# Performance work log

Measured on AMD Instinct MI355X. Metric: run time of the kernel, lower is better.

## Reference

```python
import jax, jax.numpy as jnp
import numpy as np

NMS_THRESH = 0.3  # default nms_thresh in DetNet.predict


def setup_inputs() -> dict:
    key = jax.random.key(0)
    k1, k2, k3, k4 = jax.random.split(key, 4)
    W, N = 8, 1024
    det = jax.random.uniform(k1, (W, N, 5), dtype=jnp.float32)          # (conf, cx, cy, w, h) in [0,1)
    offsets = jax.random.uniform(k2, (W, 5), dtype=jnp.float32) * 0.5   # window offset vector (0, left, top, 0, 0)-like
    scales = jax.random.uniform(k3, (W, 5), dtype=jnp.float32) * 0.5 + 0.25  # window scale vector
    b = jax.random.uniform(k4, (W, 4), dtype=jnp.float32)
    # (valid_left, valid_right, valid_top, valid_bottom) with left<right, top<bottom
    bounds = jnp.stack([0.3 * b[:, 0], 0.7 + 0.3 * b[:, 1],
                        0.3 * b[:, 2], 0.7 + 0.3 * b[:, 3]], axis=-1)
    return {"det": det, "offsets": offsets, "scales": scales, "bounds": bounds}


def _pairwise_iou(boxes):
    # boxes: [M,4] in (x1,y1,x2,y2)
    x1, y1, x2, y2 = boxes[:, 0], boxes[:, 1], boxes[:, 2], boxes[:, 3]
    area = jnp.clip(x2 - x1, 0.0) * jnp.clip(y2 - y1, 0.0)              # [M]
    iw = jnp.clip(jnp.minimum(x2[:, None], x2[None, :]) - jnp.maximum(x1[:, None], x1[None, :]), 0.0)
    ih = jnp.clip(jnp.minimum(y2[:, None], y2[None, :]) - jnp.maximum(y1[:, None], y1[None, :]), 0.0)
    inter = iw * ih                                                     # [M,M]
    union = area[:, None] + area[None, :] - inter
    return inter / jnp.maximum(union, 1e-9)


def reference(det, offsets, scales, bounds):
    W, N, _ = det.shape
    M = W * N
    cx, cy = det[..., 1], det[..., 2]                                    # [W,N]
    left, right = bounds[:, 0:1], bounds[:, 1:2]
    top, bottom = bounds[:, 2:3], bounds[:, 3:4]
    valid = (cx < right) & (cx > left) & (cy < bottom) & (cy > top)      # [W,N] border mask
    # torch.addcmul(offset, d, scale) = offset + d * scale
    d = (offsets[:, None, :] + det * scales[:, None, :]).reshape(M, 5)
    valid = valid.reshape(M)
    scores = jnp.where(valid, d[:, 0], -1.0)                             # invalid boxes never kept
    order = jnp.argsort(-scores)                                         # descending confidence
    d_s = d[order]                                                       # [M,5]
    s_s = scores[order]
    # point_form: (cx,cy,w,h) -> (x1,y1,x2,y2)
    cxy, wh = d_s[:, 1:3], d_s[:, 3:5]
    boxes = jnp.concatenate([cxy - wh * 0.5, cxy + wh * 0.5], axis=-1)
    iou = jax.lax.stop_gradient(_pairwise_iou(boxes))                    # [M,M], suppression is non-diff
    s_c = jax.lax.stop_gradient(s_s)
    idx = jnp.arange(M)

    def body(i, keep):
        # suppressed if any kept higher-score box overlaps > thresh
        sup = jnp.any(keep & (idx < i) & (iou[:, i] > NMS_THRESH))
        return keep.at[i].set(jnp.logical_and(~sup, s_c[i] > 0.0))

    keep = jax.lax.fori_loop(0, M, body, jnp.ones((M,), dtype=bool))
    return d_s * keep[:, None].astype(d_s.dtype)                         # [M,5], suppressed rows zeroed
```

## Files before the change

kernel.cpp:

```cpp
#include <hip/hip_runtime.h>
#include <cstdint>


#define M_TOT 8192
#define NMS_T 0.3f

#define WS_BOX   65536
#define WS_D     196608
#define WS_VCNT  360448
#define WS_ZROW  393216
#define WS_DONE  458752
#define WS_MASK  524288

typedef unsigned long long u64t;

__device__ __forceinline__ uint32_t desc_key(float sv) {
    uint32_t u = __float_as_uint(sv);
    uint32_t m = (u & 0x80000000u) ? ~u : (u | 0x80000000u);
    return ~m;
}
__device__ __forceinline__ u64t rdl64(u64t v, int sl) {
    unsigned lo = (unsigned)__builtin_amdgcn_readlane((int)(unsigned)v, sl);
    unsigned hi = (unsigned)__builtin_amdgcn_readlane((int)(unsigned)(v >> 32), sl);
    return ((u64t)hi << 32) | lo;
}
__device__ __forceinline__ u64t rdfl64(u64t v) {
    unsigned lo = (unsigned)__builtin_amdgcn_readfirstlane((int)(unsigned)v);
    unsigned hi = (unsigned)__builtin_amdgcn_readfirstlane((int)(unsigned)(v >> 32));
    return ((u64t)hi << 32) | lo;
}

__device__ __forceinline__ void scatter_one(
    int i, int rank, u64t key,
    const float* __restrict__ det, const float* __restrict__ offsets,
    const float* __restrict__ scales,
    float4* __restrict__ boxes_srt, float* __restrict__ d_srt)
{
    uint32_t dkey = (uint32_t)(key >> 16);
    if (dkey >= 0x7FFFFFFFu) return;
    int g = i >> 10;
    float d0 = __fadd_rn(offsets[g*5+0], __fmul_rn(det[i*5+0], scales[g*5+0]));
    float d1 = __fadd_rn(offsets[g*5+1], __fmul_rn(det[i*5+1], scales[g*5+1]));
    float d2 = __fadd_rn(offsets[g*5+2], __fmul_rn(det[i*5+2], scales[g*5+2]));
    float d3 = __fadd_rn(offsets[g*5+3], __fmul_rn(det[i*5+3], scales[g*5+3]));
    float d4 = __fadd_rn(offsets[g*5+4], __fmul_rn(det[i*5+4], scales[g*5+4]));
    d_srt[rank*5+0] = d0; d_srt[rank*5+1] = d1; d_srt[rank*5+2] = d2;
    d_srt[rank*5+3] = d3; d_srt[rank*5+4] = d4;
    float hw = __fmul_rn(d3, 0.5f), hh = __fmul_rn(d4, 0.5f);
    boxes_srt[rank] = make_float4(__fsub_rn(d1, hw), __fsub_rn(d2, hh),
                                  __fadd_rn(d1, hw), __fadd_rn(d2, hh));
}

__global__ __launch_bounds__(512) void k2_rank(
    const float* __restrict__ det, const float* __restrict__ offsets,
    const float* __restrict__ scales, const float* __restrict__ bounds,
    float4* __restrict__ boxes_srt, float* __restrict__ d_srt,
    unsigned int* __restrict__ vcnt, u64t* __restrict__ zrow,
    unsigned int* __restrict__ done, float* __restrict__ out)
{
    __shared__ u64t skey[M_TOT];
    __shared__ float soff[40], sscl[40], sbnd[32];
    __shared__ int sTop;
    int t = threadIdx.x;
    int lane = t & 63;
    if (t == 0) sTop = 0;
    if (t < 40) { soff[t] = offsets[t]; sscl[t] = scales[t]; }
    if (t < 32) { sbnd[t] = bounds[t]; }
    if (blockIdx.x == 0 && t < 128) zrow[t] = 0ull;
    if (blockIdx.x == 0 && t < 64)  done[t] = 0u;
    __syncthreads();

    #pragma unroll 4
    for (int s = 0; s < 16; ++s) {
        int u = s * 512 + t;
        int g = u >> 10;
        float raw_s = det[u * 5 + 0];
        float cx    = det[u * 5 + 1];
        float cy    = det[u * 5 + 2];
        float score = __fadd_rn(soff[g * 5 + 0], __fmul_rn(raw_s, sscl[g * 5 + 0]));
        bool valid = (cx < sbnd[g*4+1]) && (cx > sbnd[g*4+0]) &&
                     (cy < sbnd[g*4+3]) && (cy > sbnd[g*4+2]);
        float sv = valid ? score : -1.0f;
        uint32_t dk = desc_key(sv);
        bool push = dk < 0x7FFFFFFFu;
        u64t key = ((u64t)dk << 16) | (unsigned)u;
        u64t bal = __ballot(push);
        if (bal) {
            int lw = 0;
            if (lane == 0) lw = atomicAdd(&sTop, __popcll(bal));
            int wbase = __builtin_amdgcn_readfirstlane(lw);
            if (push) {
                int off = __popcll(bal & ((1ull << lane) - 1ull));
                skey[wbase + off] = key;
            }
        }
    }
    __syncthreads();
    int V = sTop;
    int Vpad = (V + 15) & ~15;
    if (t < Vpad - V) skey[V + t] = ~0ull;
    {
        int zb = blockIdx.x * 320;
        for (int z = zb + t; z < zb + 320; z += 512) out[z] = 0.0f;
    }
    __syncthreads();
    if (t == 0) *vcnt = (unsigned)V;

    int grp = t >> 3;
    int jq  = t & 7;
    int i = blockIdx.x * 64 + grp;
    int g = i >> 10;
    float raw_s = det[i * 5 + 0];
    float cx    = det[i * 5 + 1];
    float cy    = det[i * 5 + 2];
    float score = __fadd_rn(soff[g * 5 + 0], __fmul_rn(raw_s, sscl[g * 5 + 0]));
    bool valid = (cx < sbnd[g*4+1]) && (cx > sbnd[g*4+0]) &&
                 (cy < sbnd[g*4+3]) && (cy > sbnd[g*4+2]);
    float sv = valid ? score : -1.0f;
    uint32_t dk = desc_key(sv);
    u64t ki = ((u64t)dk << 16) | (unsigned)i;
    const ulonglong2* skey2 = (const ulonglong2*)skey;
    int c = 0;
    int nit = Vpad >> 4;
    #pragma unroll 4
    for (int it = 0; it < nit; ++it) {
        ulonglong2 kj = skey2[it * 8 + jq];
        c += (kj.x < ki) + (kj.y < ki);
    }
    c += __shfl_xor(c, 1);
    c += __shfl_xor(c, 2);
    c += __shfl_xor(c, 4);
    if (jq == 0)
        scatter_one(i, c, ki, det, offsets, scales, boxes_srt, d_srt);
}

__global__ __launch_bounds__(512) void k34_fused(
    const float4* __restrict__ boxes_srt,
    const u64t* __restrict__ zrow,
    const float* __restrict__ d_srt,
    const unsigned int* __restrict__ vcnt,
    u64t* __restrict__ mask,
    unsigned int* __restrict__ done,
    float* __restrict__ out)
{
    int V = (int)*vcnt;
    int nwords = (V + 63) >> 6;
    int nc = (V + 127) >> 7;
    int tid = threadIdx.x;

    if (blockIdx.x != 0) {
        __shared__ float4 sb[8 * 65];
        __shared__ float  sa[8 * 65];
        int b = (int)blockIdx.x - 1;
        int gpre = 0;
        for (int c = 0; c < nc; ++c) {
            int w0 = 2 * c;
            int Wc = nwords - w0;
            int tiles = 2 * ((Wc + 7) >> 3);
            int tau0 = ((b - gpre) % 127 + 127) % 127;
            for (int tau = tau0; tau < tiles; tau += 127) {
                int rt = tau & 1, wt = tau >> 1;
                int rowbase = c * 128 + rt * 64;
                int wbase = w0 + wt * 8;
                {
                    int u = tid;
                    float4 bb = boxes_srt[min(wbase * 64 + u, M_TOT - 1)];
                    int cc = u >> 6, jj = u & 63;
                    sb[cc * 65 + jj] = bb;
                    sa[cc * 65 + jj] = __fmul_rn(fmaxf(__fsub_rn(bb.z, bb.x), 0.0f),
                                                 fmaxf(__fsub_rn(bb.w, bb.y), 0.0f));
                }
                __syncthreads();
                int r  = rowbase + (tid >> 3);
                int wl = tid & 7;
                int w  = wbase + wl;
                if (r < V && w < nwords) {
                    float4 bi = boxes_srt[r];
                    float ai = __fmul_rn(fmaxf(__fsub_rn(bi.z, bi.x), 0.0f),
                                         fmaxf(__fsub_rn(bi.w, bi.y), 0.0f));
                    u64t bits = 0;
                    #pragma unroll 4
                    for (int jj = 0; jj < 64; ++jj) {
                        float4 bj = sb[wl * 65 + jj];
                        float aj = sa[wl * 65 + jj];
                        float iw = fmaxf(__fsub_rn(fminf(bi.z, bj.z), fmaxf(bi.x, bj.x)), 0.0f);
                        float ih = fmaxf(__fsub_rn(fminf(bi.w, bj.w), fmaxf(bi.y, bj.y)), 0.0f);
                        float inter = __fmul_rn(iw, ih);
                        float uni   = __fsub_rn(__fadd_rn(ai, aj), inter);
                        float iou   = __fdiv_rn(inter, fmaxf(uni, 1e-9f));
                        int j = w * 64 + jj;
                        if (j > r && iou > NMS_T) bits |= 1ull << jj;
                    }
                    mask[(size_t)r * 128 + w] = bits;
                }
                __syncthreads();
                if (tid == 0) {
                    int rows_t  = V - rowbase; if (rows_t > 64) rows_t = 64;
                    int words_t = nwords - wbase; if (words_t > 8) words_t = 8;
                    if (rows_t > 0) {
                        __threadfence();
                        __hip_atomic_fetch_add(&done[c], (unsigned)(rows_t * words_t),
                                               __ATOMIC_RELEASE, __HIP_MEMORY_SCOPE_AGENT);
                    }
                }
                __syncthreads();
            }
            gpre += tiles;
        }
        return;
    }

    __shared__ u64t sdead[128];
    __shared__ u64t ck[128];
    __shared__ int  res_prog;
    __shared__ int  h_prog[7];
    int wv = tid >> 6, lane = tid & 63;

    if (tid < 128) {
        int bw = tid * 64;
        u64t w0v = 0;
        if (bw >= V)           w0v = ~0ull;
        else if (bw + 64 > V)  w0v = (~0ull) << (V - bw);
        sdead[tid] = w0v;
        ck[tid] = 0ull;
    }
    if (tid == 0) res_prog = 0;
    if (tid < 7)  h_prog[tid] = tid;
    __syncthreads();

    if (wv == 0) {
        if (nc > 0) {
            u64t cA_lo = 0, cA_hi = 0;
            {
                int rows_c = V; if (rows_c > 128) rows_c = 128;
                unsigned expc = (unsigned)(rows_c * nwords);
                while (__hip_atomic_load(&done[0], __ATOMIC_RELAXED, __HIP_MEMORY_SCOPE_AGENT) < expc)
                    __builtin_amdgcn_s_sleep(2);
                (void)__hip_atomic_load(&done[0], __ATOMIC_ACQUIRE, __HIP_MEMORY_SCOPE_AGENT);
            }
            ulonglong2 bl, bln, bh, bhn;
            {
                int rl = min(lane,      M_TOT - 1);
                int rh = min(64 + lane, M_TOT - 1);
                const u64t* rpl = mask + (size_t)rl * 128;
                const u64t* rph = mask + (size_t)rh * 128;
                bl  = *(const ulonglong2*)(rpl);
                bln = *(const ulonglong2*)(rpl + 2);
                bh  = *(const ulonglong2*)(rph);
                bhn = *(const ulonglong2*)(rph + 2);
            }
            for (int T = 0; T < nc; ++T) {
                ulonglong2 nbl, nbln, nbh, nbhn;
                bool havenext = (T + 1 < nc);
                if (havenext) {
                    int c = T + 1;
                    int rows_c = V - c * 128; if (rows_c > 128) rows_c = 128;
                    unsigned expc = (unsigned)(rows_c * (nwords - 2 * c));
                    while (__hip_atomic_load(&done[c], __ATOMIC_RELAXED, __HIP_MEMORY_SCOPE_AGENT) < expc)
                        __builtin_amdgcn_s_sleep(2);
                    (void)__hip_atomic_load(&done[c], __ATOMIC_ACQUIRE, __HIP_MEMORY_SCOPE_AGENT);
                    int rl = min(c * 128 + lane,      M_TOT - 1);
                    int rh = min(c * 128 + 64 + lane, M_TOT - 1);
                    int w = min(2 * c, 124);
                    const u64t* rpl = mask + (size_t)rl * 128;
                    const u64t* rph = mask + (size_t)rh * 128;
                    nbl  = *(const ulonglong2*)(rpl + w);
                    nbln = *(const ulonglong2*)(rpl + w + 2);
                    nbh  = *(const ulonglong2*)(rph + w);
                    nbhn = *(const ulonglong2*)(rph + w + 2);
                }
                if (T >= 2) {
                    int need = T - 1;
                    while (true) {
                        int hp = (lane < 7) ? ((volatile int*)h_prog)[lane] : 0x7FFFFFFF;
                        if (__ballot(hp < need) == 0ull) break;
                    }
                }
                u64t dlo = rdfl64(((volatile u64t*)sdead)[2 * T]);
                u64t dhi = rdfl64(((volatile u64t*)sdead)[2 * T + 1]);
                u64t live_lo = ~(dlo | cA_lo);
                u64t live_hi = ~(dhi | cA_hi);
                int rem = V - T * 128;
                if (rem < 128) {
                    live_lo &= (rem >= 64) ? ~0ull : ((rem <= 0) ? 0ull : ((1ull << rem) - 1ull));
                    int rh = rem - 64;
                    live_hi &= (rh >= 64) ? ~0ull : ((rh <= 0) ? 0ull : ((1ull << rh) - 1ull));
                }
                u64t km_lo = 0, km_hi = 0;
                while (live_lo) {
                    int bs = (int)__builtin_ctzll(live_lo);
                    km_lo |= 1ull << bs;
                    u64t rml = rdl64(bl.x, bs);
                    u64t rmh = rdl64(bl.y, bs);
                    live_lo &= ~rml & ~(1ull << bs);
                    live_hi &= ~rmh;
                }
                while (live_hi) {
                    int bs = (int)__builtin_ctzll(live_hi);
                    km_hi |= 1ull << bs;
                    u64t rmh = rdl64(bh.y, bs);
                    live_hi &= ~rmh & ~(1ull << bs);
                }
                if (lane == 0) { ck[2 * T] = km_lo; ck[2 * T + 1] = km_hi; }
                __threadfence_block();
                if (lane == 0) *(volatile int*)&res_prog = T + 1;
                u64t c1l = 0, c1h = 0, km = km_lo;
                while (km) {
                    int b_ = (int)__builtin_ctzll(km); km &= km - 1;
                    c1l |= rdl64(bln.x, b_); c1h |= rdl64(bln.y, b_);
                }
                km = km_hi;
                while (km) {
                    int b_ = (int)__builtin_ctzll(km); km &= km - 1;
                    c1l |= rdl64(bhn.x, b_); c1h |= rdl64(bhn.y, b_);
                }
                cA_lo = c1l; cA_hi = c1h;
                if (havenext) { bl = nbl; bln = nbln; bh = nbh; bhn = nbhn; }
            }
        }
    } else {
        int hh = wv - 1;
        for (int c = hh; c < nc; c += 7) {
            while (*(volatile int*)&res_prog <= c) __builtin_amdgcn_s_sleep(1);
            (void)__hip_atomic_load(&done[c], __ATOMIC_ACQUIRE, __HIP_MEMORY_SCOPE_AGENT);
            u64t kl = ((volatile u64t*)ck)[2 * c];
            u64t kh = ((volatile u64t*)ck)[2 * c + 1];
            if (kl | kh) {
                int base = c * 128;
                u64t ax = 0, ay = 0;
                while (kl | kh) {
                    ulonglong2 bq[4];
                    #pragma unroll
                    for (int q = 0; q < 4; ++q) {
                        const ulonglong2* ptr;
                        if (kl) {
                            int b_ = __builtin_ctzll(kl); kl &= kl - 1;
                            ptr = (const ulonglong2*)(mask + (size_t)(base + b_) * 128) + lane;
                        } else if (kh) {
                            int b_ = __builtin_ctzll(kh); kh &= kh - 1;
                            ptr = (const ulonglong2*)(mask + (size_t)(base + 64 + b_) * 128) + lane;
                        } else {
                            ptr = (const ulonglong2*)zrow + lane;
                        }
                        bq[q] = *ptr;
                    }
                    ax |= bq[0].x | bq[1].x | bq[2].x | bq[3].x;
                    ay |= bq[0].y | bq[1].y | bq[2].y | bq[3].y;
                }
                atomicOr(&sdead[2 * lane],     ax);
                atomicOr(&sdead[2 * lane + 1], ay);
            }
            __threadfence_block();
            if (lane == 0) ((volatile int*)h_prog)[hh] = c + 7;
        }
        if (lane == 0) ((volatile int*)h_prog)[hh] = 0x7FFFFFFF;
    }
    __syncthreads();
    if (tid < 128) {
        u64t m = ck[tid];
        while (m) {
            int b_ = __builtin_ctzll(m); m &= m - 1;
            int rr = tid * 64 + b_;
            out[rr * 5 + 0] = d_srt[rr * 5 + 0];
            out[rr * 5 + 1] = d_srt[rr * 5 + 1];
            out[rr * 5 + 2] = d_srt[rr * 5 + 2];
            out[rr * 5 + 3] = d_srt[rr * 5 + 3];
            out[rr * 5 + 4] = d_srt[rr * 5 + 4];
        }
    }
}

extern "C" void kernel_launch(void* const* d_in, const int* in_sizes, int n_in,
                              void* d_out, int out_size, void* d_ws, size_t ws_size,
                              hipStream_t stream) {
    const float* det     = (const float*)d_in[0];
    const float* offsets = (const float*)d_in[1];
    const float* scales  = (const float*)d_in[2];
    const float* bounds  = (const float*)d_in[3];
    float* out = (float*)d_out;
    char* ws = (char*)d_ws;
    float4*       boxes = (float4*)(ws + WS_BOX);
    float*        d_srt = (float*)(ws + WS_D);
    unsigned int* vcnt  = (unsigned int*)(ws + WS_VCNT);
    u64t*         zrow  = (u64t*)(ws + WS_ZROW);
    unsigned int* done  = (unsigned int*)(ws + WS_DONE);
    u64t*         mask  = (u64t*)(ws + WS_MASK);

    k2_rank<<<128, 512, 0, stream>>>(det, offsets, scales, bounds, boxes, d_srt, vcnt, zrow, done, out);
    k34_fused<<<128, 512, 0, stream>>>(boxes, zrow, d_srt, vcnt, mask, done, out);
}
```

Before: 138.7 us.

## Build diagonal mask tiles first and signal them with separate per-chunk counters

Worker blocks now compute the diagonal (wt==0) mask tiles for every chunk before any off-diagonal tiles. Each diagonal tile bumps a new doneD counter, so the resolver wave only waits on diagonal completion instead of the whole chunk row. The helper waves that OR suppression rows now spin on the full done counter themselves. This lets the serial resolve chain start earlier and overlap with off-diagonal mask construction, at the cost of extra atomics and a changed tile schedule.

```diff
diff --git a/kernel.cpp b/kernel.cpp
--- a/kernel.cpp
+++ b/kernel.cpp
@@ -10,6 +10,7 @@
 #define WS_VCNT  360448
 #define WS_ZROW  393216
 #define WS_DONE  458752
+#define WS_DONED 459008
 #define WS_MASK  524288
 
 typedef unsigned long long u64t;
@@ -56,7 +57,8 @@
     const float* __restrict__ scales, const float* __restrict__ bounds,
     float4* __restrict__ boxes_srt, float* __restrict__ d_srt,
     unsigned int* __restrict__ vcnt, u64t* __restrict__ zrow,
-    unsigned int* __restrict__ done, float* __restrict__ out)
+    unsigned int* __restrict__ done, unsigned int* __restrict__ doneD,
+    float* __restrict__ out)
 {
     __shared__ u64t skey[M_TOT];
     __shared__ float soff[40], sscl[40], sbnd[32];
@@ -67,7 +69,7 @@
     if (t < 40) { soff[t] = offsets[t]; sscl[t] = scales[t]; }
     if (t < 32) { sbnd[t] = bounds[t]; }
     if (blockIdx.x == 0 && t < 128) zrow[t] = 0ull;
-    if (blockIdx.x == 0 && t < 64)  done[t] = 0u;
+    if (blockIdx.x == 0 && t < 64)  { done[t] = 0u; doneD[t] = 0u; }
     __syncthreads();
 
     #pragma unroll 4
@@ -134,6 +136,61 @@
         scatter_one(i, c, ki, det, offsets, scales, boxes_srt, d_srt);
 }
 
+__device__ __forceinline__ void build_tile(
+    int c, int rt, int wt, int V, int nwords,
+    const float4* __restrict__ boxes_srt, u64t* __restrict__ mask,
+    unsigned int* __restrict__ done, unsigned int* __restrict__ doneD,
+    float4* sb, float* sa, int tid)
+{
+    int rowbase = c * 128 + rt * 64;
+    int wbase = 2 * c + wt * 8;
+    {
+        int u = tid;
+        float4 bb = boxes_srt[min(wbase * 64 + u, M_TOT - 1)];
+        int cc = u >> 6, jj = u & 63;
+        sb[cc * 65 + jj] = bb;
+        sa[cc * 65 + jj] = __fmul_rn(fmaxf(__fsub_rn(bb.z, bb.x), 0.0f),
+                                     fmaxf(__fsub_rn(bb.w, bb.y), 0.0f));
+    }
+    __syncthreads();
+    int r  = rowbase + (tid >> 3);
+    int wl = tid & 7;
+    int w  = wbase + wl;
+    if (r < V && w < nwords) {
+        float4 bi = boxes_srt[r];
+        float ai = __fmul_rn(fmaxf(__fsub_rn(bi.z, bi.x), 0.0f),
+                             fmaxf(__fsub_rn(bi.w, bi.y), 0.0f));
+        u64t bits = 0;
+        #pragma unroll 4
+        for (int jj = 0; jj < 64; ++jj) {
+            float4 bj = sb[wl * 65 + jj];
+            float aj = sa[wl * 65 + jj];
+            float iw = fmaxf(__fsub_rn(fminf(bi.z, bj.z), fmaxf(bi.x, bj.x)), 0.0f);
+            float ih = fmaxf(__fsub_rn(fminf(bi.w, bj.w), fmaxf(bi.y, bj.y)), 0.0f);
+            float inter = __fmul_rn(iw, ih);
+            float uni   = __fsub_rn(__fadd_rn(ai, aj), inter);
+            float iou   = __fdiv_rn(inter, fmaxf(uni, 1e-9f));
+            int j = w * 64 + jj;
+            if (j > r && iou > NMS_T) bits |= 1ull << jj;
+        }
+        mask[(size_t)r * 128 + w] = bits;
+    }
+    __syncthreads();
+    if (tid == 0) {
+        int rows_t  = V - rowbase; if (rows_t > 64) rows_t = 64;
+        int words_t = nwords - wbase; if (words_t > 8) words_t = 8;
+        if (rows_t > 0) {
+            __threadfence();
+            __hip_atomic_fetch_add(&done[c], (unsigned)(rows_t * words_t),
+                                   __ATOMIC_RELEASE, __HIP_MEMORY_SCOPE_AGENT);
+            if (wt == 0)
+                __hip_atomic_fetch_add(&doneD[c], 1u,
+                                       __ATOMIC_RELEASE, __HIP_MEMORY_SCOPE_AGENT);
+        }
+    }
+    __syncthreads();
+}
+
 __global__ __launch_bounds__(512) void k34_fused(
     const float4* __restrict__ boxes_srt,
     const u64t* __restrict__ zrow,
@@ -141,6 +198,7 @@
     const unsigned int* __restrict__ vcnt,
     u64t* __restrict__ mask,
     unsigned int* __restrict__ done,
+    unsigned int* __restrict__ doneD,
     float* __restrict__ out)
 {
     int V = (int)*vcnt;
@@ -152,58 +210,19 @@
         __shared__ float4 sb[8 * 65];
         __shared__ float  sa[8 * 65];
         int b = (int)blockIdx.x - 1;
+        for (int d = b; d < 2 * nc; d += 127) {
+            build_tile(d >> 1, d & 1, 0, V, nwords,
+                       boxes_srt, mask, done, doneD, sb, sa, tid);
+        }
         int gpre = 0;
         for (int c = 0; c < nc; ++c) {
-            int w0 = 2 * c;
-            int Wc = nwords - w0;
-            int tiles = 2 * ((Wc + 7) >> 3);
+            int Wc = nwords - 2 * c;
+            int octets = (Wc + 7) >> 3;
+            int tiles = 2 * (octets - 1);
             int tau0 = ((b - gpre) % 127 + 127) % 127;
             for (int tau = tau0; tau < tiles; tau += 127) {
-                int rt = tau & 1, wt = tau >> 1;
-                int rowbase = c * 128 + rt * 64;
-                int wbase = w0 + wt * 8;
-                {
-                    int u = tid;
-                    float4 bb = boxes_srt[min(wbase * 64 + u, M_TOT - 1)];
-                    int cc = u >> 6, jj = u & 63;
-                    sb[cc * 65 + jj] = bb;
-                    sa[cc * 65 + jj] = __fmul_rn(fmaxf(__fsub_rn(bb.z, bb.x), 0.0f),
-                                                 fmaxf(__fsub_rn(bb.w, bb.y), 0.0f));
-                }
-                __syncthreads();
-                int r  = rowbase + (tid >> 3);
-                int wl = tid & 7;
-                int w  = wbase + wl;
-                if (r < V && w < nwords) {
-                    float4 bi = boxes_srt[r];
-                    float ai = __fmul_rn(fmaxf(__fsub_rn(bi.z, bi.x), 0.0f),
-                                         fmaxf(__fsub_rn(bi.w, bi.y), 0.0f));
-                    u64t bits = 0;
-                    #pragma unroll 4
-                    for (int jj = 0; jj < 64; ++jj) {
-                        float4 bj = sb[wl * 65 + jj];
-                        float aj = sa[wl * 65 + jj];
-                        float iw = fmaxf(__fsub_rn(fminf(bi.z, bj.z), fmaxf(bi.x, bj.x)), 0.0f);
-                        float ih = fmaxf(__fsub_rn(fminf(bi.w, bj.w), fmaxf(bi.y, bj.y)), 0.0f);
-                        float inter = __fmul_rn(iw, ih);
-                        float uni   = __fsub_rn(__fadd_rn(ai, aj), inter);
-                        float iou   = __fdiv_rn(inter, fmaxf(uni, 1e-9f));
-                        int j = w * 64 + jj;
-                        if (j > r && iou > NMS_T) bits |= 1ull << jj;
-                    }
-                    mask[(size_t)r * 128 + w] = bits;
-                }
-                __syncthreads();
-                if (tid == 0) {
-                    int rows_t  = V - rowbase; if (rows_t > 64) rows_t = 64;
-                    int words_t = nwords - wbase; if (words_t > 8) words_t = 8;
-                    if (rows_t > 0) {
-                        __threadfence();
-                        __hip_atomic_fetch_add(&done[c], (unsigned)(rows_t * words_t),
-                                               __ATOMIC_RELEASE, __HIP_MEMORY_SCOPE_AGENT);
-                    }
-                }
-                __syncthreads();
+                build_tile(c, tau & 1, (tau >> 1) + 1, V, nwords,
+                           boxes_srt, mask, done, doneD, sb, sa, tid);
             }
             gpre += tiles;
         }
@@ -233,10 +252,10 @@
             u64t cA_lo = 0, cA_hi = 0;
             {
                 int rows_c = V; if (rows_c > 128) rows_c = 128;
-                unsigned expc = (unsigned)(rows_c * nwords);
-                while (__hip_atomic_load(&done[0], __ATOMIC_RELAXED, __HIP_MEMORY_SCOPE_AGENT) < expc)
+                unsigned expd = (rows_c > 64) ? 2u : 1u;
+                while (__hip_atomic_load(&doneD[0], __ATOMIC_RELAXED, __HIP_MEMORY_SCOPE_AGENT) < expd)
                     __builtin_amdgcn_s_sleep(2);
-                (void)__hip_atomic_load(&done[0], __ATOMIC_ACQUIRE, __HIP_MEMORY_SCOPE_AGENT);
+                (void)__hip_atomic_load(&doneD[0], __ATOMIC_ACQUIRE, __HIP_MEMORY_SCOPE_AGENT);
             }
             ulonglong2 bl, bln, bh, bhn;
             {
@@ -255,10 +274,10 @@
                 if (havenext) {
                     int c = T + 1;
                     int rows_c = V - c * 128; if (rows_c > 128) rows_c = 128;
-                    unsigned expc = (unsigned)(rows_c * (nwords - 2 * c));
-                    while (__hip_atomic_load(&done[c], __ATOMIC_RELAXED, __HIP_MEMORY_SCOPE_AGENT) < expc)
+                    unsigned expd = (rows_c > 64) ? 2u : 1u;
+                    while (__hip_atomic_load(&doneD[c], __ATOMIC_RELAXED, __HIP_MEMORY_SCOPE_AGENT) < expd)
                         __builtin_amdgcn_s_sleep(2);
-                    (void)__hip_atomic_load(&done[c], __ATOMIC_ACQUIRE, __HIP_MEMORY_SCOPE_AGENT);
+                    (void)__hip_atomic_load(&doneD[c], __ATOMIC_ACQUIRE, __HIP_MEMORY_SCOPE_AGENT);
                     int rl = min(c * 128 + lane,      M_TOT - 1);
                     int rh = min(c * 128 + 64 + lane, M_TOT - 1);
                     int w = min(2 * c, 124);
@@ -322,7 +341,13 @@
         int hh = wv - 1;
         for (int c = hh; c < nc; c += 7) {
             while (*(volatile int*)&res_prog <= c) __builtin_amdgcn_s_sleep(1);
-            (void)__hip_atomic_load(&done[c], __ATOMIC_ACQUIRE, __HIP_MEMORY_SCOPE_AGENT);
+            {
+                int rows_c = V - c * 128; if (rows_c > 128) rows_c = 128;
+                unsigned expc = (unsigned)(rows_c * (nwords - 2 * c));
+                while (__hip_atomic_load(&done[c], __ATOMIC_RELAXED, __HIP_MEMORY_SCOPE_AGENT) < expc)
+                    __builtin_amdgcn_s_sleep(1);
+                (void)__hip_atomic_load(&done[c], __ATOMIC_ACQUIRE, __HIP_MEMORY_SCOPE_AGENT);
+            }
             u64t kl = ((volatile u64t*)ck)[2 * c];
             u64t kh = ((volatile u64t*)ck)[2 * c + 1];
             if (kl | kh) {
@@ -384,8 +409,11 @@
     unsigned int* vcnt  = (unsigned int*)(ws + WS_VCNT);
     u64t*         zrow  = (u64t*)(ws + WS_ZROW);
     unsigned int* done  = (unsigned int*)(ws + WS_DONE);
+    unsigned int* doneD = (unsigned int*)(ws + WS_DONED);
     u64t*         mask  = (u64t*)(ws + WS_MASK);
 
-    k2_rank<<<128, 512, 0, stream>>>(det, offsets, scales, bounds, boxes, d_srt, vcnt, zrow, done, out);
-    k34_fused<<<128, 512, 0, stream>>>(boxes, zrow, d_srt, vcnt, mask, done, out);
-}
+    k2_rank<<<128, 512, 0, stream>>>(det, offsets, scales, bounds, boxes, d_srt,
+                                     vcnt, zrow, done, doneD, out);
+    k34_fused<<<dim3(128), 512, 0, stream>>>(boxes, zrow, d_srt, vcnt, mask,
+                                             done, doneD, out);
+}
```

Result: slower. 144.6 us (+4.2%).

## Replace multi-wave NMS resolve pipeline with single-wave register-resident dead mask

Applied to the files above, without the earlier changes.

The serial NMS resolve stage moves from a one-resolver-plus-seven-helper-wavefront scheme, which coordinated through shared memory progress flags and atomics, to a single wavefront. That wavefront keeps the accumulated suppression bitmask in registers (two u64 per lane) and ORs in the mask rows of kept boxes itself. Output rows for kept boxes are written inline, so the final block-wide scatter pass is gone. This removes cross-wave spin-waiting, LDS atomics and the early next-tile lookahead (cA), at the cost of making the resolver wave do all mask-row loads serially on its critical path.

```diff
diff --git a/kernel.cpp b/kernel.cpp
--- a/kernel.cpp
+++ b/kernel.cpp
@@ -22,11 +22,6 @@
 __device__ __forceinline__ u64t rdl64(u64t v, int sl) {
     unsigned lo = (unsigned)__builtin_amdgcn_readlane((int)(unsigned)v, sl);
     unsigned hi = (unsigned)__builtin_amdgcn_readlane((int)(unsigned)(v >> 32), sl);
-    return ((u64t)hi << 32) | lo;
-}
-__device__ __forceinline__ u64t rdfl64(u64t v) {
-    unsigned lo = (unsigned)__builtin_amdgcn_readfirstlane((int)(unsigned)v);
-    unsigned hi = (unsigned)__builtin_amdgcn_readfirstlane((int)(unsigned)(v >> 32));
     return ((u64t)hi << 32) | lo;
 }
 
@@ -210,163 +205,91 @@
         return;
     }
 
-    __shared__ u64t sdead[128];
-    __shared__ u64t ck[128];
-    __shared__ int  res_prog;
-    __shared__ int  h_prog[7];
-    int wv = tid >> 6, lane = tid & 63;
-
-    if (tid < 128) {
-        int bw = tid * 64;
-        u64t w0v = 0;
-        if (bw >= V)           w0v = ~0ull;
-        else if (bw + 64 > V)  w0v = (~0ull) << (V - bw);
-        sdead[tid] = w0v;
-        ck[tid] = 0ull;
-    }
-    if (tid == 0) res_prog = 0;
-    if (tid < 7)  h_prog[tid] = tid;
-    __syncthreads();
-
-    if (wv == 0) {
-        if (nc > 0) {
-            u64t cA_lo = 0, cA_hi = 0;
-            {
-                int rows_c = V; if (rows_c > 128) rows_c = 128;
-                unsigned expc = (unsigned)(rows_c * nwords);
-                while (__hip_atomic_load(&done[0], __ATOMIC_RELAXED, __HIP_MEMORY_SCOPE_AGENT) < expc)
-                    __builtin_amdgcn_s_sleep(2);
-                (void)__hip_atomic_load(&done[0], __ATOMIC_ACQUIRE, __HIP_MEMORY_SCOPE_AGENT);
+    if (tid >= 64) return;
+    int lane = tid;
+    if (nc <= 0) return;
+
+    u64t dr0 = 0, dr1 = 0;
+
+    {
+        int rows_c = V; if (rows_c > 128) rows_c = 128;
+        unsigned expc = (unsigned)(rows_c * nwords);
+        while (__hip_atomic_load(&done[0], __ATOMIC_RELAXED, __HIP_MEMORY_SCOPE_AGENT) < expc)
+            __builtin_amdgcn_s_sleep(2);
+        (void)__hip_atomic_load(&done[0], __ATOMIC_ACQUIRE, __HIP_MEMORY_SCOPE_AGENT);
+    }
+    ulonglong2 bl, bh;
+    {
+        int rl = min(lane,      M_TOT - 1);
+        int rh = min(64 + lane, M_TOT - 1);
+        bl = *((const ulonglong2*)(mask + (size_t)rl * 128));
+        bh = *((const ulonglong2*)(mask + (size_t)rh * 128));
+    }
+    for (int T = 0; T < nc; ++T) {
+        ulonglong2 nbl, nbh;
+        bool havenext = (T + 1 < nc);
+        if (havenext) {
+            int c = T + 1;
+            int rows_c = V - c * 128; if (rows_c > 128) rows_c = 128;
+            unsigned expc = (unsigned)(rows_c * (nwords - 2 * c));
+            while (__hip_atomic_load(&done[c], __ATOMIC_RELAXED, __HIP_MEMORY_SCOPE_AGENT) < expc)
+                __builtin_amdgcn_s_sleep(2);
+            (void)__hip_atomic_load(&done[c], __ATOMIC_ACQUIRE, __HIP_MEMORY_SCOPE_AGENT);
+            int rl = min(c * 128 + lane,      M_TOT - 1);
+            int rh = min(c * 128 + 64 + lane, M_TOT - 1);
+            int w = min(2 * c, 124);
+            nbl = *((const ulonglong2*)(mask + (size_t)rl * 128 + w));
+            nbh = *((const ulonglong2*)(mask + (size_t)rh * 128 + w));
+        }
+        u64t dlo = rdl64(dr0, T);
+        u64t dhi = rdl64(dr1, T);
+        u64t live_lo = ~dlo;
+        u64t live_hi = ~dhi;
+        int rem = V - T * 128;
+        if (rem < 128) {
+            live_lo &= (rem >= 64) ? ~0ull : ((rem <= 0) ? 0ull : ((1ull << rem) - 1ull));
+            int rh = rem - 64;
+            live_hi &= (rh >= 64) ? ~0ull : ((rh <= 0) ? 0ull : ((1ull << rh) - 1ull));
+        }
+        u64t km_lo = 0, km_hi = 0;
+        while (live_lo) {
+            int bs = (int)__builtin_ctzll(live_lo);
+            km_lo |= 1ull << bs;
+            u64t rml = rdl64(bl.x, bs);
+            u64t rmh = rdl64(bl.y, bs);
+            live_lo &= ~rml & ~(1ull << bs);
+            live_hi &= ~rmh;
+        }
+        while (live_hi) {
+            int bs = (int)__builtin_ctzll(live_hi);
+            km_hi |= 1ull << bs;
+            u64t rmh = rdl64(bh.y, bs);
+            live_hi &= ~rmh & ~(1ull << bs);
+        }
+        {
+            int base = T * 128;
+            u64t ka = km_lo, kb = km_hi;
+            while (ka | kb) {
+                int r0, r1 = -1;
+                if (ka) { int b_ = (int)__builtin_ctzll(ka); ka &= ka - 1; r0 = base + b_; }
+                else    { int b_ = (int)__builtin_ctzll(kb); kb &= kb - 1; r0 = base + 64 + b_; }
+                if (ka)      { int b_ = (int)__builtin_ctzll(ka); ka &= ka - 1; r1 = base + b_; }
+                else if (kb) { int b_ = (int)__builtin_ctzll(kb); kb &= kb - 1; r1 = base + 64 + b_; }
+                const ulonglong2* p0 = (const ulonglong2*)(mask + (size_t)r0 * 128) + lane;
+                const ulonglong2* p1 = (r1 >= 0)
+                    ? (const ulonglong2*)(mask + (size_t)r1 * 128) + lane
+                    : (const ulonglong2*)zrow + lane;
+                ulonglong2 v0 = *p0;
+                ulonglong2 v1 = *p1;
+                dr0 |= v0.x | v1.x;
+                dr1 |= v0.y | v1.y;
+                if (lane < 5) {
+                    out[r0 * 5 + lane] = d_srt[r0 * 5 + lane];
+                    if (r1 >= 0) out[r1 * 5 + lane] = d_srt[r1 * 5 + lane];
+                }
             }
-            ulonglong2 bl, bln, bh, bhn;
-            {
-                int rl = min(lane,      M_TOT - 1);
-                int rh = min(64 + lane, M_TOT - 1);
-                const u64t* rpl = mask + (size_t)rl * 128;
-                const u64t* rph = mask + (size_t)rh * 128;
-                bl  = *(const ulonglong2*)(rpl);
-                bln = *(const ulonglong2*)(rpl + 2);
-                bh  = *(const ulonglong2*)(rph);
-                bhn = *(const ulonglong2*)(rph + 2);
-            }
-            for (int T = 0; T < nc; ++T) {
-                ulonglong2 nbl, nbln, nbh, nbhn;
-                bool havenext = (T + 1 < nc);
-                if (havenext) {
-                    int c = T + 1;
-                    int rows_c = V - c * 128; if (rows_c > 128) rows_c = 128;
-                    unsigned expc = (unsigned)(rows_c * (nwords - 2 * c));
-                    while (__hip_atomic_load(&done[c], __ATOMIC_RELAXED, __HIP_MEMORY_SCOPE_AGENT) < expc)
-                        __builtin_amdgcn_s_sleep(2);
-                    (void)__hip_atomic_load(&done[c], __ATOMIC_ACQUIRE, __HIP_MEMORY_SCOPE_AGENT);
-                    int rl = min(c * 128 + lane,      M_TOT - 1);
-                    int rh = min(c * 128 + 64 + lane, M_TOT - 1);
-                    int w = min(2 * c, 124);
-                    const u64t* rpl = mask + (size_t)rl * 128;
-                    const u64t* rph = mask + (size_t)rh * 128;
-                    nbl  = *(const ulonglong2*)(rpl + w);
-                    nbln = *(const ulonglong2*)(rpl + w + 2);
-                    nbh  = *(const ulonglong2*)(rph + w);
-                    nbhn = *(const ulonglong2*)(rph + w + 2);
-                }
-                if (T >= 2) {
-                    int need = T - 1;
-                    while (true) {
-                        int hp = (lane < 7) ? ((volatile int*)h_prog)[lane] : 0x7FFFFFFF;
-                        if (__ballot(hp < need) == 0ull) break;
-                    }
-                }
-                u64t dlo = rdfl64(((volatile u64t*)sdead)[2 * T]);
-                u64t dhi = rdfl64(((volatile u64t*)sdead)[2 * T + 1]);
-                u64t live_lo = ~(dlo | cA_lo);
-                u64t live_hi = ~(dhi | cA_hi);
-                int rem = V - T * 128;
-                if (rem < 128) {
-                    live_lo &= (rem >= 64) ? ~0ull : ((rem <= 0) ? 0ull : ((1ull << rem) - 1ull));
-                    int rh = rem - 64;
-                    live_hi &= (rh >= 64) ? ~0ull : ((rh <= 0) ? 0ull : ((1ull << rh) - 1ull));
-                }
-                u64t km_lo = 0, km_hi = 0;
-                while (live_lo) {
-                    int bs = (int)__builtin_ctzll(live_lo);
-                    km_lo |= 1ull << bs;
-                    u64t rml = rdl64(bl.x, bs);
-                    u64t rmh = rdl64(bl.y, bs);
-                    live_lo &= ~rml & ~(1ull << bs);
-                    live_hi &= ~rmh;
-                }
-                while (live_hi) {
-                    int bs = (int)__builtin_ctzll(live_hi);
-                    km_hi |= 1ull << bs;
-                    u64t rmh = rdl64(bh.y, bs);
-                    live_hi &= ~rmh & ~(1ull << bs);
-                }
-                if (lane == 0) { ck[2 * T] = km_lo; ck[2 * T + 1] = km_hi; }
-                __threadfence_block();
-                if (lane == 0) *(volatile int*)&res_prog = T + 1;
-                u64t c1l = 0, c1h = 0, km = km_lo;
-                while (km) {
-                    int b_ = (int)__builtin_ctzll(km); km &= km - 1;
-                    c1l |= rdl64(bln.x, b_); c1h |= rdl64(bln.y, b_);
-                }
-                km = km_hi;
-                while (km) {
-                    int b_ = (int)__builtin_ctzll(km); km &= km - 1;
-                    c1l |= rdl64(bhn.x, b_); c1h |= rdl64(bhn.y, b_);
-                }
-                cA_lo = c1l; cA_hi = c1h;
-                if (havenext) { bl = nbl; bln = nbln; bh = nbh; bhn = nbhn; }
-            }
-        }
-    } else {
-        int hh = wv - 1;
-        for (int c = hh; c < nc; c += 7) {
-            while (*(volatile int*)&res_prog <= c) __builtin_amdgcn_s_sleep(1);
-            (void)__hip_atomic_load(&done[c], __ATOMIC_ACQUIRE, __HIP_MEMORY_SCOPE_AGENT);
-            u64t kl = ((volatile u64t*)ck)[2 * c];
-            u64t kh = ((volatile u64t*)ck)[2 * c + 1];
-            if (kl | kh) {
-                int base = c * 128;
-                u64t ax = 0, ay = 0;
-                while (kl | kh) {
-                    ulonglong2 bq[4];
-                    #pragma unroll
-                    for (int q = 0; q < 4; ++q) {
-                        const ulonglong2* ptr;
-                        if (kl) {
-                            int b_ = __builtin_ctzll(kl); kl &= kl - 1;
-                            ptr = (const ulonglong2*)(mask + (size_t)(base + b_) * 128) + lane;
-                        } else if (kh) {
-                            int b_ = __builtin_ctzll(kh); kh &= kh - 1;
-                            ptr = (const ulonglong2*)(mask + (size_t)(base + 64 + b_) * 128) + lane;
-                        } else {
-                            ptr = (const ulonglong2*)zrow + lane;
-                        }
-                        bq[q] = *ptr;
-                    }
-                    ax |= bq[0].x | bq[1].x | bq[2].x | bq[3].x;
-                    ay |= bq[0].y | bq[1].y | bq[2].y | bq[3].y;
-                }
-                atomicOr(&sdead[2 * lane],     ax);
-                atomicOr(&sdead[2 * lane + 1], ay);
-            }
-            __threadfence_block();
-            if (lane == 0) ((volatile int*)h_prog)[hh] = c + 7;
-        }
-        if (lane == 0) ((volatile int*)h_prog)[hh] = 0x7FFFFFFF;
-    }
-    __syncthreads();
-    if (tid < 128) {
-        u64t m = ck[tid];
-        while (m) {
-            int b_ = __builtin_ctzll(m); m &= m - 1;
-            int rr = tid * 64 + b_;
-            out[rr * 5 + 0] = d_srt[rr * 5 + 0];
-            out[rr * 5 + 1] = d_srt[rr * 5 + 1];
-            out[rr * 5 + 2] = d_srt[rr * 5 + 2];
-            out[rr * 5 + 3] = d_srt[rr * 5 + 3];
-            out[rr * 5 + 4] = d_srt[rr * 5 + 4];
-        }
+        }
+        if (havenext) { bl = nbl; bh = nbh; }
     }
 }
 
@@ -386,6 +309,7 @@
     unsigned int* done  = (unsigned int*)(ws + WS_DONE);
     u64t*         mask  = (u64t*)(ws + WS_MASK);
 
-    k2_rank<<<128, 512, 0, stream>>>(det, offsets, scales, bounds, boxes, d_srt, vcnt, zrow, done, out);
+    k2_rank<<<128, 512, 0, stream>>>(det, offsets, scales, bounds, boxes, d_srt,
+                                     vcnt, zrow, done, out);
     k34_fused<<<128, 512, 0, stream>>>(boxes, zrow, d_srt, vcnt, mask, done, out);
 }
```

Measured after the change: 155.6 us. +12.1%, slower.
